# Kernel optimization log

Hardware: AMD Instinct MI355X
Metric: run time of the kernel (lower is better)

The kernel has to match this reference:

```python
import jax, jax.numpy as jnp
from jax import lax
import numpy as np

B, T, C, H, K = 16, 1024, 1024, 16, 31
PAD = K // 2


def setup_inputs() -> dict:
    key = jax.random.key(0)
    ks = jax.random.split(key, 10)
    inp = {
        "query": jax.random.normal(ks[0], (B, T, C), jnp.float32),
        "key": jax.random.normal(ks[1], (B, T, C), jnp.float32),
        "value": jax.random.normal(ks[2], (B, T, C), jnp.float32),
        "mask": jnp.ones((B, 1, T), jnp.int32),
        # linear1: n_feat -> 2*n_feat ; linear2: 2*n_feat -> n_feat (torch Linear convention W:(out,in))
        "W1": jax.random.normal(ks[3], (2 * C, C), jnp.float32) / np.sqrt(C),
        "b1": jnp.zeros((2 * C,), jnp.float32),
        "W2": jax.random.normal(ks[4], (C, 2 * C), jnp.float32) / np.sqrt(2 * C),
        "b2": jnp.zeros((C,), jnp.float32),
        # shared depthwise kernels, uniform(0,1) as in the torch init
        "weight": jax.random.uniform(ks[5], (H, 1, K), jnp.float32),
        "weight_f": jax.random.uniform(ks[6], (1, 1, K), jnp.float32),
    }
    return inp


def reference(query, key, value, mask, W1, b1, W2, b2, weight, weight_f):
    # eval mode: dropout is identity (dropout_rate irrelevant); use_kernel_mask=False, use_bias=False
    x = query @ W1.T + b1                      # (B,T,2C)
    a, g = jnp.split(x, 2, axis=-1)
    x = a * jax.nn.sigmoid(g)                  # GLU -> (B,T,C)

    dn = ("NCH", "OIH", "NCH")
    # 2D branch: conv along the FEATURE axis with a single softmax-normalized kernel,
    # shared across all (b,t) positions (the torch code replicates weight_f B*T times).
    wf = jax.nn.softmax(weight_f, axis=-1)     # (1,1,K)
    xf = lax.conv_general_dilated(
        x.reshape(B * T, 1, C), wf, (1,), [(PAD, PAD)], dimension_numbers=dn
    ).reshape(B, T, C)

    # time branch: depthwise conv over time, kernel shared across C//H channels per head.
    # channel c uses head h = c % H (from view(-1, H, T) on contiguous (B,C,T)).
    w = jax.nn.softmax(weight, axis=-1)        # (H,1,K)
    xt = x.transpose(0, 2, 1).reshape(B * (C // H), H, T)
    xc = lax.conv_general_dilated(
        xt, w, (1,), [(PAD, PAD)], dimension_numbers=dn, feature_group_count=H
    ).reshape(B, C, T).transpose(0, 2, 1)      # (B,T,C)

    x = jnp.concatenate([xc, xf], axis=-1)     # (B,T,2C)
    m = jnp.transpose(mask, (0, 2, 1))         # (B,T,1)
    x = jnp.where(m == 0, 0.0, x)
    return x @ W2.T + b2                       # (B,T,C)
```

## Files before the change

kernel.cpp:

```cpp
#include <hip/hip_runtime.h>
#include <hip/hip_bf16.h>

#define B_  16
#define T_  1024
#define C_  1024
#define H_  16
#define KW_ 31
#define M_  (B_ * T_)
#define N1_ (2 * C_)
#define K1_ C_
#define N2_ C_
#define K2_ (2 * C_)

typedef __attribute__((ext_vector_type(8))) short bf16x8;
typedef __attribute__((ext_vector_type(4))) short s16x4;
typedef __attribute__((ext_vector_type(4))) float f32x4;

typedef const __attribute__((address_space(1))) void GV;
typedef __attribute__((address_space(3))) void LV;

__device__ __forceinline__ short f2bf(float f) {
  union { float f; unsigned u; } v; v.f = f;
  unsigned r = v.u + 0x7fffu + ((v.u >> 16) & 1u);
  return (short)(r >> 16);
}
__device__ __forceinline__ float b2f(short s) {
  union { float f; unsigned u; } v;
  v.u = ((unsigned)(unsigned short)s) << 16;
  return v.f;
}

__global__ void softmax_w(const float* __restrict__ w,
                          const float* __restrict__ wf,
                          float* __restrict__ wsm) {
  int t = threadIdx.x;
  if (t >= 17) return;
  const float* src = (t < 16) ? (w + t * KW_) : wf;
  float mx = -1e30f;
  #pragma unroll
  for (int k = 0; k < KW_; ++k) mx = fmaxf(mx, src[k]);
  float e[KW_], s = 0.f;
  #pragma unroll
  for (int k = 0; k < KW_; ++k) { e[k] = __expf(src[k] - mx); s += e[k]; }
  float inv = 1.f / s;
  #pragma unroll
  for (int k = 0; k < KW_; ++k) wsm[t * KW_ + k] = e[k] * inv;
}

__global__ void cvt_bf16(const float* __restrict__ in, short* __restrict__ out, int n4) {
  int i = blockIdx.x * blockDim.x + threadIdx.x;
  if (i >= n4) return;
  float4 f = ((const float4*)in)[i];
  s16x4 s = { f2bf(f.x), f2bf(f.y), f2bf(f.z), f2bf(f.w) };
  ((s16x4*)out)[i] = s;
}

__global__ void cvt_w1i(const float* __restrict__ W1, short* __restrict__ W1b) {
  int idx = blockIdx.x * blockDim.x + threadIdx.x;
  int r = idx >> 7;
  int c = (idx & 127) * 8;
  int s = (r & 1) ? (1024 + (r >> 1)) : (r >> 1);
  const float* src = W1 + (long)s * 1024 + c;
  bf16x8 o;
  #pragma unroll
  for (int i = 0; i < 8; ++i) o[i] = f2bf(src[i]);
  *(bf16x8*)(W1b + (long)r * 1024 + c) = o;
}

__global__ void cvt_w2c(const float* __restrict__ W2, short* __restrict__ W2b) {
  int i = blockIdx.x * blockDim.x + threadIdx.x;
  int o  = i >> 8;
  int c4 = (i & 255) * 4;
  float4 f = *(const float4*)(W2 + (long)o * K2_ + c4);
  s16x4 s = { f2bf(f.x), f2bf(f.y), f2bf(f.z), f2bf(f.w) };
  *(s16x4*)(W2b + (long)o * K2_ + c4) = s;
}

__global__ void fold_w2f(const float* __restrict__ W2,
                         const float* __restrict__ wsm,
                         short* __restrict__ W2b) {
  int idx = blockIdx.x * blockDim.x + threadIdx.x;
  int o = idx >> 10, j = idx & 1023;
  const float* base = W2 + (long)o * K2_ + C_;
  float s = 0.f;
  #pragma unroll
  for (int k = 0; k < KW_; ++k) {
    int c = j + 15 - k;
    if (c >= 0 && c < C_) s += wsm[16 * KW_ + k] * base[c];
  }
  W2b[(long)o * K2_ + C_ + j] = f2bf(s);
}

__global__ __launch_bounds__(256) void conv_t_k(const short* __restrict__ A2in,
                                                const float* __restrict__ wsm,
                                                short* __restrict__ A2out) {
  const int tid = threadIdx.x;
  const int t0  = blockIdx.x * 128;
  const int c   = blockIdx.y * 256 + tid;
  const int b   = blockIdx.z;
  const int h   = c & (H_ - 1);

  float wk[KW_];
  #pragma unroll
  for (int k = 0; k < KW_; ++k) wk[k] = wsm[h * KW_ + k];

  const long rowbase = ((long)b * T_) * K2_ + C_ + c;
  float win[KW_];
  #pragma unroll
  for (int k = 0; k < 30; ++k) {
    int t = t0 - 15 + k;
    win[k] = (t >= 0 && t < T_) ? b2f(A2in[rowbase + (long)t * K2_]) : 0.f;
  }
  for (int tt = 0; tt < 128; ++tt) {
    int tl = t0 + tt + 15;
    win[30] = (tl < T_) ? b2f(A2in[rowbase + (long)tl * K2_]) : 0.f;
    float s = 0.f;
    #pragma unroll
    for (int k = 0; k < KW_; ++k) s = fmaf(wk[k], win[k], s);
    A2out[((long)b * T_ + t0 + tt) * K2_ + c] = f2bf(s);
    #pragma unroll
    for (int k = 0; k < 30; ++k) win[k] = win[k + 1];
  }
}


#define ST_H(GP, GR0, BUFS, REG, KT, HH) do { \
    int d = tid * 16;                   \
    int rr_ = (HH) * 64 + (d >> 7);     \
    int scb = (d & 127) ^ ((rr_ & 7) << 4); \
    __builtin_amdgcn_global_load_lds( \
      (GV*)(GP + (long)(GR0 + rr_) * K + (KT) * 64 + (scb >> 1)), \
      (LV*)&lds[(BUFS) + (REG) + (HH) * 4096 + (d >> 1)], 16, 0, 0); \
  } while (0)
#define ST_A(BUFS, KT) do { ST_H(A,  arow0, BUFS, 0,    KT, 0); \
                            ST_H(A,  arow0, BUFS, 0,    KT, 1); } while (0)
#define ST_B(BUFS, KT) do { ST_H(Bw, brow0, BUFS, 8192, KT, 0); \
                            ST_H(Bw, brow0, BUFS, 8192, KT, 1); } while (0)

#define RD_A2(DST, BUFS, MP) do { \
    _Pragma("unroll") \
    for (int mm = 0; mm < 2; ++mm) \
      _Pragma("unroll") \
      for (int kk = 0; kk < 2; ++kk) { \
        int r = wm * 64 + ((MP) * 2 + mm) * 16 + rlane; \
        int byt = (r * 128 + kk * 64 + klb) ^ ((r & 7) << 4); \
        DST[mm * 2 + kk] = *(const bf16x8*)&lds[(BUFS) + (byt >> 1)]; \
      } \
  } while (0)

#define RD_B(DST, BUFS) do { \
    _Pragma("unroll") \
    for (int n = 0; n < 2; ++n) \
      _Pragma("unroll") \
      for (int kk = 0; kk < 2; ++kk) { \
        int r = wn * 32 + n * 16 + rlane; \
        int byt = (r * 128 + kk * 64 + klb) ^ ((r & 7) << 4); \
        DST[n * 2 + kk] = *(const bf16x8*)&lds[(BUFS) + 8192 + (byt >> 1)]; \
      } \
  } while (0)

#define MM(AV, BV, MP) do { \
    _Pragma("unroll") \
    for (int mm = 0; mm < 2; ++mm) \
      _Pragma("unroll") \
      for (int n = 0; n < 2; ++n) \
        _Pragma("unroll") \
        for (int kk = 0; kk < 2; ++kk) \
          acc[2 * (MP) + mm][n] = __builtin_amdgcn_mfma_f32_16x16x32_bf16( \
              AV[mm * 2 + kk], BV[n * 2 + kk], acc[2 * (MP) + mm][n], 0, 0, 0); \
  } while (0)

#define VMW(n_)  asm volatile("s_waitcnt vmcnt(" #n_ ")" ::: "memory")
#define BARO() do { asm volatile("" ::: "memory"); __builtin_amdgcn_s_barrier(); \
                    __builtin_amdgcn_s_setprio(1); } while (0)
#define BARC() do { __builtin_amdgcn_s_setprio(0); \
                    asm volatile("" ::: "memory"); __builtin_amdgcn_s_barrier(); \
                    asm volatile("" ::: "memory"); } while (0)

template<int MODE>
__global__ __launch_bounds__(512, 4) void gemm128(const short* __restrict__ A,
                                                  const short* __restrict__ Bw,
                                                  const float* __restrict__ bias,
                                                  void* __restrict__ Cout,
                                                  int K, int NBN, int ldo) {
  __shared__ short lds[32768];
  const int tid  = threadIdx.x;
  const int lane = tid & 63;
  const int wave = tid >> 6;
  const int wm = wave >> 2, wn = wave & 3;

  const int nwg = gridDim.x;
  const int wg  = (blockIdx.x & 7) * (nwg >> 3) + (blockIdx.x >> 3);
  const int bm = wg / NBN, bn = wg % NBN;
  const int arow0 = bm * 128, brow0 = bn * 128;

  const int rlane = lane & 15;
  const int klb   = (lane >> 4) * 16;

  f32x4 acc[4][2] = {};
  const int nt = K >> 6;
  const int ni = nt >> 1;

  bf16x8 aF[4], bA[4], bB[4];

  ST_A(0, 0); ST_B(0, 0);
  ST_B(16384, 1);
  VMW(2);
  asm volatile("" ::: "memory"); __builtin_amdgcn_s_barrier();

  for (int i = 0; i + 1 < ni; ++i) {
    const int kt1 = 2 * i + 1, kt2 = 2 * i + 2, kt3 = 2 * i + 3;
     RD_B(bA, 0); RD_A2(aF, 0, 0);         ST_A(16384, kt1);          BARO(); MM(aF, bA, 0); BARC();
     RD_A2(aF, 0, 1);                      ST_B(0, kt2);     VMW(2);  BARO(); MM(aF, bA, 1); BARC();
     RD_B(bB, 16384); RD_A2(aF, 16384, 0); ST_A(0, kt2);              BARO(); MM(aF, bB, 0); BARC();
     RD_A2(aF, 16384, 1);                  ST_B(16384, kt3); VMW(2);  BARO(); MM(aF, bB, 1); BARC();
  }
   RD_B(bA, 0); RD_A2(aF, 0, 0);           ST_A(16384, nt - 1);       BARO(); MM(aF, bA, 0); BARC();
   RD_A2(aF, 0, 1);                                           VMW(0); BARO(); MM(aF, bA, 1); BARC();
   RD_B(bB, 16384); RD_A2(aF, 16384, 0);                              BARO(); MM(aF, bB, 0); BARC();
   RD_A2(aF, 16384, 1);                                               BARO(); MM(aF, bB, 1);
  __builtin_amdgcn_s_setprio(0);

  #pragma unroll
  for (int m = 0; m < 4; ++m) {
    const int r = arow0 + wm * 64 + m * 16 + (lane >> 4) * 4;
    #pragma unroll
    for (int n = 0; n < 2; ++n) {
      const int c = brow0 + wn * 32 + n * 16 + (lane & 15);
      if (MODE == 0) {
        const float bb = bias[c];
        #pragma unroll
        for (int i = 0; i < 4; ++i)
          ((float*)Cout)[(long)(r + i) * ldo + c] = acc[m][n][i] + bb;
      } else {
        const int oc = (c & 1) ? (1024 + (c >> 1)) : (c >> 1);
        const float bb = bias[oc];
        #pragma unroll
        for (int i = 0; i < 4; ++i) {
          float v = acc[m][n][i] + bb;
          float o = __shfl_xor(v, 1);
          if (!(c & 1))
            ((short*)Cout)[(long)(r + i) * ldo + 1024 + (c >> 1)] =
                f2bf(v / (1.f + __expf(-o)));
        }
      }
    }
  }
}

extern "C" void kernel_launch(void* const* d_in, const int* in_sizes, int n_in,
                              void* d_out, int out_size, void* d_ws, size_t ws_size,
                              hipStream_t stream) {
  const float* q   = (const float*)d_in[0];
  const float* W1  = (const float*)d_in[4];
  const float* b1  = (const float*)d_in[5];
  const float* W2  = (const float*)d_in[6];
  const float* b2  = (const float*)d_in[7];
  const float* wt  = (const float*)d_in[8];
  const float* wtf = (const float*)d_in[9];

  short* Abf = (short*)d_ws;
  short* W1b = Abf + (long)M_ * K1_;
  short* W2b = W1b + (long)N1_ * K1_;
  short* A2  = W2b + (long)N2_ * K2_;
  float* wsm = (float*)(A2 + (long)M_ * K2_);

  softmax_w<<<1, 64, 0, stream>>>(wt, wtf, wsm);

  cvt_bf16<<<(M_ * K1_ / 4) / 256, 256, 0, stream>>>(q, Abf, M_ * K1_ / 4);
  cvt_w1i<<<(N1_ * K1_ / 8) / 256, 256, 0, stream>>>(W1, W1b);
  cvt_w2c<<<(C_ * C_ / 4) / 256, 256, 0, stream>>>(W2, W2b);
  fold_w2f<<<(C_ * C_) / 256, 256, 0, stream>>>(W2, wsm, W2b);

  gemm128<1><<<(M_ / 128) * (N1_ / 128), 512, 0, stream>>>(
      Abf, W1b, b1, A2, K1_, N1_ / 128, K2_);

  conv_t_k<<<dim3(T_ / 128, C_ / 256, B_), 256, 0, stream>>>(A2, wsm, A2);

  gemm128<0><<<(M_ / 128) * (N2_ / 128), 512, 0, stream>>>(
      A2, W2b, b2, d_out, K2_, N2_ / 128, N2_);
}
```

Measured before the change: 239.1 us.

## Restructure GEMM to 4-wave blocks with 64x64 warp tiles and BK=32

The GEMM kernel moves from 8 waves (each computing a 64x32 output slice) to 4 waves (each computing 64x64), with the K step per stage halved from 64 to 32 and LDS shrunk to 32 KB. The XOR swizzle on LDS addresses is dropped and the prefetch order changes to alternate A and B halves. The aim is higher MFMA-to-LDS-read ratio per wave and lower LDS footprint for better occupancy. In exchange it loses the bank-conflict swizzle, adds twice as many barriers per K, and raises accumulator register pressure.

```diff
diff --git a/kernel.cpp b/kernel.cpp
--- a/kernel.cpp
+++ b/kernel.cpp
@@ -124,50 +124,41 @@
 }
 
 
-#define ST_H(GP, GR0, BUFS, REG, KT, HH) do { \
-    int d = tid * 16;                   \
-    int rr_ = (HH) * 64 + (d >> 7);     \
-    int scb = (d & 127) ^ ((rr_ & 7) << 4); \
-    __builtin_amdgcn_global_load_lds( \
-      (GV*)(GP + (long)(GR0 + rr_) * K + (KT) * 64 + (scb >> 1)), \
-      (LV*)&lds[(BUFS) + (REG) + (HH) * 4096 + (d >> 1)], 16, 0, 0); \
-  } while (0)
-#define ST_A(BUFS, KT) do { ST_H(A,  arow0, BUFS, 0,    KT, 0); \
-                            ST_H(A,  arow0, BUFS, 0,    KT, 1); } while (0)
-#define ST_B(BUFS, KT) do { ST_H(Bw, brow0, BUFS, 8192, KT, 0); \
-                            ST_H(Bw, brow0, BUFS, 8192, KT, 1); } while (0)
-
-#define RD_A2(DST, BUFS, MP) do { \
-    _Pragma("unroll") \
-    for (int mm = 0; mm < 2; ++mm) \
+#define ST_R(GP, GR0, BUFS, REG, KT) do { \
+    _Pragma("unroll") \
+    for (int i = 0; i < 2; ++i) { \
+      int d = i * 4096 + tid * 16;    \
+      __builtin_amdgcn_global_load_lds( \
+        (GV*)(GP + (long)(GR0 + (d >> 6)) * K + (KT) * 32 + ((d & 63) >> 1)), \
+        (LV*)&lds[(BUFS) + (REG) + (d >> 1)], 16, 0, 0); \
+    } \
+  } while (0)
+#define ST_A(BUFS, KT) ST_R(A,  arow0, BUFS, 0,    KT)
+#define ST_B(BUFS, KT) ST_R(Bw, brow0, BUFS, 4096, KT)
+
+#define RD_A(BUFS) do { \
+    _Pragma("unroll") \
+    for (int mf = 0; mf < 4; ++mf) { \
+      int r = wm * 64 + mf * 16 + rlane; \
+      aF[mf] = *(const bf16x8*)&lds[(BUFS) + ((r * 64 + klb) >> 1)]; \
+    } \
+  } while (0)
+
+#define RD_B(DST, BUFS, NP) do { \
+    _Pragma("unroll") \
+    for (int j = 0; j < 2; ++j) { \
+      int r = wn * 64 + (NP) * 32 + j * 16 + rlane; \
+      DST[j] = *(const bf16x8*)&lds[(BUFS) + 4096 + ((r * 64 + klb) >> 1)]; \
+    } \
+  } while (0)
+
+#define MM(BV, NP) do { \
+    _Pragma("unroll") \
+    for (int mf = 0; mf < 4; ++mf) \
       _Pragma("unroll") \
-      for (int kk = 0; kk < 2; ++kk) { \
-        int r = wm * 64 + ((MP) * 2 + mm) * 16 + rlane; \
-        int byt = (r * 128 + kk * 64 + klb) ^ ((r & 7) << 4); \
-        DST[mm * 2 + kk] = *(const bf16x8*)&lds[(BUFS) + (byt >> 1)]; \
-      } \
-  } while (0)
-
-#define RD_B(DST, BUFS) do { \
-    _Pragma("unroll") \
-    for (int n = 0; n < 2; ++n) \
-      _Pragma("unroll") \
-      for (int kk = 0; kk < 2; ++kk) { \
-        int r = wn * 32 + n * 16 + rlane; \
-        int byt = (r * 128 + kk * 64 + klb) ^ ((r & 7) << 4); \
-        DST[n * 2 + kk] = *(const bf16x8*)&lds[(BUFS) + 8192 + (byt >> 1)]; \
-      } \
-  } while (0)
-
-#define MM(AV, BV, MP) do { \
-    _Pragma("unroll") \
-    for (int mm = 0; mm < 2; ++mm) \
-      _Pragma("unroll") \
-      for (int n = 0; n < 2; ++n) \
-        _Pragma("unroll") \
-        for (int kk = 0; kk < 2; ++kk) \
-          acc[2 * (MP) + mm][n] = __builtin_amdgcn_mfma_f32_16x16x32_bf16( \
-              AV[mm * 2 + kk], BV[n * 2 + kk], acc[2 * (MP) + mm][n], 0, 0, 0); \
+      for (int j = 0; j < 2; ++j) \
+        acc[mf][(NP) * 2 + j] = __builtin_amdgcn_mfma_f32_16x16x32_bf16( \
+            aF[mf], BV[j], acc[mf][(NP) * 2 + j], 0, 0, 0); \
   } while (0)
 
 #define VMW(n_)  asm volatile("s_waitcnt vmcnt(" #n_ ")" ::: "memory")
@@ -178,16 +169,16 @@
                     asm volatile("" ::: "memory"); } while (0)
 
 template<int MODE>
-__global__ __launch_bounds__(512, 4) void gemm128(const short* __restrict__ A,
-                                                  const short* __restrict__ Bw,
-                                                  const float* __restrict__ bias,
-                                                  void* __restrict__ Cout,
-                                                  int K, int NBN, int ldo) {
-  __shared__ short lds[32768];
+__global__ __launch_bounds__(256, 4) void gemm_bal(const short* __restrict__ A,
+                                                   const short* __restrict__ Bw,
+                                                   const float* __restrict__ bias,
+                                                   void* __restrict__ Cout,
+                                                   int K, int NBN, int ldo) {
+  __shared__ short lds[16384];
   const int tid  = threadIdx.x;
   const int lane = tid & 63;
   const int wave = tid >> 6;
-  const int wm = wave >> 2, wn = wave & 3;
+  const int wm = wave >> 1, wn = wave & 1;
 
   const int nwg = gridDim.x;
   const int wg  = (blockIdx.x & 7) * (nwg >> 3) + (blockIdx.x >> 3);
@@ -197,36 +188,36 @@
   const int rlane = lane & 15;
   const int klb   = (lane >> 4) * 16;
 
-  f32x4 acc[4][2] = {};
-  const int nt = K >> 6;
+  f32x4 acc[4][4] = {};
+  const int nt = K >> 5;
   const int ni = nt >> 1;
 
-  bf16x8 aF[4], bA[4], bB[4];
+  bf16x8 aF[4], bF[2], bG[2];
 
   ST_A(0, 0); ST_B(0, 0);
-  ST_B(16384, 1);
+  ST_A(8192, 1);
   VMW(2);
   asm volatile("" ::: "memory"); __builtin_amdgcn_s_barrier();
 
   for (int i = 0; i + 1 < ni; ++i) {
     const int kt1 = 2 * i + 1, kt2 = 2 * i + 2, kt3 = 2 * i + 3;
-     RD_B(bA, 0); RD_A2(aF, 0, 0);         ST_A(16384, kt1);          BARO(); MM(aF, bA, 0); BARC();
-     RD_A2(aF, 0, 1);                      ST_B(0, kt2);     VMW(2);  BARO(); MM(aF, bA, 1); BARC();
-     RD_B(bB, 16384); RD_A2(aF, 16384, 0); ST_A(0, kt2);              BARO(); MM(aF, bB, 0); BARC();
-     RD_A2(aF, 16384, 1);                  ST_B(16384, kt3); VMW(2);  BARO(); MM(aF, bB, 1); BARC();
-  }
-   RD_B(bA, 0); RD_A2(aF, 0, 0);           ST_A(16384, nt - 1);       BARO(); MM(aF, bA, 0); BARC();
-   RD_A2(aF, 0, 1);                                           VMW(0); BARO(); MM(aF, bA, 1); BARC();
-   RD_B(bB, 16384); RD_A2(aF, 16384, 0);                              BARO(); MM(aF, bB, 0); BARC();
-   RD_A2(aF, 16384, 1);                                               BARO(); MM(aF, bB, 1);
+     RD_A(0);    RD_B(bF, 0, 0);    ST_B(8192, kt1);          BARO(); MM(bF, 0); BARC();
+     RD_B(bG, 0, 1);                ST_A(0, kt2);     VMW(2); BARO(); MM(bG, 1); BARC();
+     RD_A(8192); RD_B(bF, 8192, 0); ST_B(0, kt2);             BARO(); MM(bF, 0); BARC();
+     RD_B(bG, 8192, 1);             ST_A(8192, kt3);  VMW(2); BARO(); MM(bG, 1); BARC();
+  }
+   RD_A(0);    RD_B(bF, 0, 0);      ST_B(8192, nt - 1);       BARO(); MM(bF, 0); BARC();
+   RD_B(bG, 0, 1);                                    VMW(0); BARO(); MM(bG, 1); BARC();
+   RD_A(8192); RD_B(bF, 8192, 0);                             BARO(); MM(bF, 0); BARC();
+   RD_B(bG, 8192, 1);                                         BARO(); MM(bG, 1);
   __builtin_amdgcn_s_setprio(0);
 
   #pragma unroll
   for (int m = 0; m < 4; ++m) {
     const int r = arow0 + wm * 64 + m * 16 + (lane >> 4) * 4;
     #pragma unroll
-    for (int n = 0; n < 2; ++n) {
-      const int c = brow0 + wn * 32 + n * 16 + (lane & 15);
+    for (int n = 0; n < 4; ++n) {
+      const int c = brow0 + wn * 64 + n * 16 + (lane & 15);
       if (MODE == 0) {
         const float bb = bias[c];
         #pragma unroll
@@ -272,11 +263,11 @@
   cvt_w2c<<<(C_ * C_ / 4) / 256, 256, 0, stream>>>(W2, W2b);
   fold_w2f<<<(C_ * C_) / 256, 256, 0, stream>>>(W2, wsm, W2b);
 
-  gemm128<1><<<(M_ / 128) * (N1_ / 128), 512, 0, stream>>>(
+  gemm_bal<1><<<(M_ / 128) * (N1_ / 128), 256, 0, stream>>>(
       Abf, W1b, b1, A2, K1_, N1_ / 128, K2_);
 
   conv_t_k<<<dim3(T_ / 128, C_ / 256, B_), 256, 0, stream>>>(A2, wsm, A2);
 
-  gemm128<0><<<(M_ / 128) * (N2_ / 128), 512, 0, stream>>>(
+  gemm_bal<0><<<(M_ / 128) * (N2_ / 128), 256, 0, stream>>>(
       A2, W2b, b2, d_out, K2_, N2_ / 128, N2_);
 }
```

Measured after the change: 264.4 us. +10.6%, slower.

## Load GEMM B fragments straight from global into registers, staging only A in LDS

Applied to the files above, without the earlier changes.

The B operand tile is no longer staged through LDS. Each wave loads its own B MFMA fragments directly from global memory into registers, double-buffered in even and odd register sets. LDS shrinks to half the size, holding only the double-buffered A tile, and the wait counts become full drains. This removes the LDS writes and reads for B and may raise occupancy, but each wave now issues uncoalesced, per-wave-redundant global loads for B (the four waves sharing a wn column load the same data) and waits with vmcnt(0) every half-step.

```diff
diff --git a/kernel.cpp b/kernel.cpp
--- a/kernel.cpp
+++ b/kernel.cpp
@@ -124,18 +124,15 @@
 }
 
 
-#define ST_H(GP, GR0, BUFS, REG, KT, HH) do { \
+#define ST_H(BUFS, KT, HH) do { \
     int d = tid * 16;                   \
     int rr_ = (HH) * 64 + (d >> 7);     \
     int scb = (d & 127) ^ ((rr_ & 7) << 4); \
     __builtin_amdgcn_global_load_lds( \
-      (GV*)(GP + (long)(GR0 + rr_) * K + (KT) * 64 + (scb >> 1)), \
-      (LV*)&lds[(BUFS) + (REG) + (HH) * 4096 + (d >> 1)], 16, 0, 0); \
-  } while (0)
-#define ST_A(BUFS, KT) do { ST_H(A,  arow0, BUFS, 0,    KT, 0); \
-                            ST_H(A,  arow0, BUFS, 0,    KT, 1); } while (0)
-#define ST_B(BUFS, KT) do { ST_H(Bw, brow0, BUFS, 8192, KT, 0); \
-                            ST_H(Bw, brow0, BUFS, 8192, KT, 1); } while (0)
+      (GV*)(A + (long)(arow0 + rr_) * K + (KT) * 64 + (scb >> 1)), \
+      (LV*)&lds[(BUFS) + (HH) * 4096 + (d >> 1)], 16, 0, 0); \
+  } while (0)
+#define ST_A(BUFS, KT) do { ST_H(BUFS, KT, 0); ST_H(BUFS, KT, 1); } while (0)
 
 #define RD_A2(DST, BUFS, MP) do { \
     _Pragma("unroll") \
@@ -148,15 +145,11 @@
       } \
   } while (0)
 
-#define RD_B(DST, BUFS) do { \
-    _Pragma("unroll") \
-    for (int n = 0; n < 2; ++n) \
-      _Pragma("unroll") \
-      for (int kk = 0; kk < 2; ++kk) { \
-        int r = wn * 32 + n * 16 + rlane; \
-        int byt = (r * 128 + kk * 64 + klb) ^ ((r & 7) << 4); \
-        DST[n * 2 + kk] = *(const bf16x8*)&lds[(BUFS) + 8192 + (byt >> 1)]; \
-      } \
+#define LD_B(DST, KT) do { \
+    DST[0] = *(const bf16x8*)(bl0 + (long)(KT) * 64); \
+    DST[1] = *(const bf16x8*)(bl0 + (long)(KT) * 64 + 32); \
+    DST[2] = *(const bf16x8*)(bl1 + (long)(KT) * 64); \
+    DST[3] = *(const bf16x8*)(bl1 + (long)(KT) * 64 + 32); \
   } while (0)
 
 #define MM(AV, BV, MP) do { \
@@ -183,7 +176,7 @@
                                                   const float* __restrict__ bias,
                                                   void* __restrict__ Cout,
                                                   int K, int NBN, int ldo) {
-  __shared__ short lds[32768];
+  __shared__ short lds[16384];
   const int tid  = threadIdx.x;
   const int lane = tid & 63;
   const int wave = tid >> 6;
@@ -197,28 +190,31 @@
   const int rlane = lane & 15;
   const int klb   = (lane >> 4) * 16;
 
+  const short* bl0 = Bw + (long)(brow0 + wn * 32 + rlane) * K + (lane >> 4) * 8;
+  const short* bl1 = bl0 + (long)16 * K;
+
   f32x4 acc[4][2] = {};
   const int nt = K >> 6;
   const int ni = nt >> 1;
 
-  bf16x8 aF[4], bA[4], bB[4];
-
-  ST_A(0, 0); ST_B(0, 0);
-  ST_B(16384, 1);
-  VMW(2);
+  bf16x8 aF[4], bE[4], bO[4];
+
+  LD_B(bE, 0);
+  ST_A(0, 0);
+  VMW(0);
   asm volatile("" ::: "memory"); __builtin_amdgcn_s_barrier();
 
   for (int i = 0; i + 1 < ni; ++i) {
-    const int kt1 = 2 * i + 1, kt2 = 2 * i + 2, kt3 = 2 * i + 3;
-     RD_B(bA, 0); RD_A2(aF, 0, 0);         ST_A(16384, kt1);          BARO(); MM(aF, bA, 0); BARC();
-     RD_A2(aF, 0, 1);                      ST_B(0, kt2);     VMW(2);  BARO(); MM(aF, bA, 1); BARC();
-     RD_B(bB, 16384); RD_A2(aF, 16384, 0); ST_A(0, kt2);              BARO(); MM(aF, bB, 0); BARC();
-     RD_A2(aF, 16384, 1);                  ST_B(16384, kt3); VMW(2);  BARO(); MM(aF, bB, 1); BARC();
-  }
-   RD_B(bA, 0); RD_A2(aF, 0, 0);           ST_A(16384, nt - 1);       BARO(); MM(aF, bA, 0); BARC();
-   RD_A2(aF, 0, 1);                                           VMW(0); BARO(); MM(aF, bA, 1); BARC();
-   RD_B(bB, 16384); RD_A2(aF, 16384, 0);                              BARO(); MM(aF, bB, 0); BARC();
-   RD_A2(aF, 16384, 1);                                               BARO(); MM(aF, bB, 1);
+    const int kt1 = 2 * i + 1, kt2 = 2 * i + 2;
+     RD_A2(aF, 0, 0);    LD_B(bO, kt1); ST_A(8192, kt1); BARO(); MM(aF, bE, 0); BARC();
+     RD_A2(aF, 0, 1);    VMW(0);                         BARO(); MM(aF, bE, 1); BARC();
+     RD_A2(aF, 8192, 0); LD_B(bE, kt2); ST_A(0, kt2);    BARO(); MM(aF, bO, 0); BARC();
+     RD_A2(aF, 8192, 1); VMW(0);                         BARO(); MM(aF, bO, 1); BARC();
+  }
+   RD_A2(aF, 0, 0);    LD_B(bO, nt - 1); ST_A(8192, nt - 1); BARO(); MM(aF, bE, 0); BARC();
+   RD_A2(aF, 0, 1);    VMW(0);                               BARO(); MM(aF, bE, 1); BARC();
+   RD_A2(aF, 8192, 0);                                       BARO(); MM(aF, bO, 0); BARC();
+   RD_A2(aF, 8192, 1);                                       BARO(); MM(aF, bO, 1);
   __builtin_amdgcn_s_setprio(0);
 
   #pragma unroll
```

New measurement: 395.9 us. 1.66x slower.
